# Optimization experiments

Hardware: AMD Instinct MI355X
Metric: run time of the kernel (lower is better)

## Reference

```python
import jax, jax.numpy as jnp
import numpy as np

DIM = 3072
HEADS = 24
HD = 128  # head_dim
RANK = 64
COND = 1024      # (512//8)*(512//8)*16//64
BLOCK = 2048     # main latent tokens
SEQ = BLOCK + COND
NIP = 64         # image_emb tokens
LORA_W = 1.0     # lora_weights[0]
ALPHA_SCALE = 1.0  # network_alpha / rank = 64/64
IP_SCALE = 1.0


def setup_inputs() -> dict:
    key = jax.random.key(0)
    ks = jax.random.split(key, 21)
    d = {}
    d["hidden_states"] = jax.random.normal(ks[0], (1, SEQ, DIM), jnp.float32)
    d["image_emb"] = jax.random.normal(ks[1], (1, NIP, DIM), jnp.float32)
    d["rope_cos"] = jax.random.uniform(ks[2], (SEQ, HD), jnp.float32)
    d["rope_sin"] = jax.random.uniform(ks[3], (SEQ, HD), jnp.float32)
    d["wq"] = jax.random.normal(ks[4], (DIM, DIM), jnp.float32) * 0.02
    d["bq"] = jax.random.normal(ks[5], (DIM,), jnp.float32) * 0.02
    d["wk"] = jax.random.normal(ks[6], (DIM, DIM), jnp.float32) * 0.02
    d["bk"] = jax.random.normal(ks[7], (DIM,), jnp.float32) * 0.02
    d["wv"] = jax.random.normal(ks[8], (DIM, DIM), jnp.float32) * 0.02
    d["bv"] = jax.random.normal(ks[9], (DIM,), jnp.float32) * 0.02
    d["norm_q_w"] = jax.random.uniform(ks[10], (HD,), jnp.float32, 0.5, 1.5)
    d["norm_k_w"] = jax.random.uniform(ks[11], (HD,), jnp.float32, 0.5, 1.5)
    d["q_down"] = jax.random.normal(ks[12], (RANK, DIM), jnp.float32) / RANK
    d["q_up"] = jax.random.normal(ks[13], (DIM, RANK), jnp.float32) * 0.02
    d["k_down"] = jax.random.normal(ks[14], (RANK, DIM), jnp.float32) / RANK
    d["k_up"] = jax.random.normal(ks[15], (DIM, RANK), jnp.float32) * 0.02
    d["v_down"] = jax.random.normal(ks[16], (RANK, DIM), jnp.float32) / RANK
    d["v_up"] = jax.random.normal(ks[17], (DIM, RANK), jnp.float32) * 0.02
    d["wk_ip"] = jax.random.normal(ks[18], (DIM, DIM), jnp.float32) * 0.02
    d["wv_ip"] = jax.random.normal(ks[19], (DIM, DIM), jnp.float32) * 0.02
    return d


def _rmsnorm(x, w, eps):
    v = jnp.mean(jnp.square(x), axis=-1, keepdims=True)
    y = x * jax.lax.rsqrt(v + eps)
    return y if w is None else y * w


def _heads(x, b):  # (B,S,DIM) -> (B,H,S,HD)
    return x.reshape(b, -1, HEADS, HD).transpose(0, 2, 1, 3)


def _rope(x, cos, sin):
    # diffusers apply_rotary_emb, use_real, unbind_dim=-1
    x1 = x[..., 0::2]
    x2 = x[..., 1::2]
    rot = jnp.stack([-x2, x1], axis=-1).reshape(x.shape)
    return x * cos[None, None] + rot * sin[None, None]


def _sdpa(q, k, v, bias=None):
    s = jnp.einsum("bhqd,bhkd->bhqk", q, k) / jnp.sqrt(jnp.float32(q.shape[-1]))
    if bias is not None:
        s = s + bias
    p = jax.nn.softmax(s, axis=-1)
    return jnp.einsum("bhqk,bhkd->bhqd", p, v)


def reference(hidden_states, image_emb, rope_cos, rope_sin,
              wq, bq, wk, bk, wv, bv, norm_q_w, norm_k_w,
              q_down, q_up, k_down, k_up, v_down, v_up, wk_ip, wv_ip):
    B = hidden_states.shape[0]

    # base QKV projections
    q = hidden_states @ wq.T + bq
    k = hidden_states @ wk.T + bk
    v = hidden_states @ wv.T + bv

    # original (pre-LoRA, pre-norm, pre-RoPE) query on the main block for IP attention
    original_query = _heads(hidden_states[:, :BLOCK] @ wq.T + bq, B)

    # masked LoRA add (n_loras=1): only tokens [BLOCK, BLOCK+COND) contribute
    pos = jnp.arange(SEQ)
    tok_mask = ((pos >= BLOCK) & (pos < BLOCK + COND)).astype(hidden_states.dtype)
    hm = hidden_states * tok_mask[None, :, None]
    q = q + LORA_W * ALPHA_SCALE * ((hm @ q_down.T) @ q_up.T)
    k = k + LORA_W * ALPHA_SCALE * ((hm @ k_down.T) @ k_up.T)
    v = v + LORA_W * ALPHA_SCALE * ((hm @ v_down.T) @ v_up.T)

    q = _heads(q, B)
    k = _heads(k, B)
    v = _heads(v, B)

    # per-head RMSNorm (attn.norm_q / attn.norm_k, eps=1e-6 in Flux)
    q = _rmsnorm(q, norm_q_w, 1e-6)
    k = _rmsnorm(k, norm_k_w, 1e-6)

    # IP-adapter cross attention with the original query
    ip_k = _rmsnorm(_heads(image_emb @ wk_ip.T, B), None, 1e-5)
    ip_v = _heads(image_emb @ wv_ip.T, B)
    ip_out = _sdpa(original_query, ip_k, ip_v)  # (B,H,BLOCK,HD)
    ip_out = ip_out.transpose(0, 2, 1, 3).reshape(B, -1, DIM)

    # RoPE on q/k
    q = _rope(q, rope_cos, rope_sin)
    k = _rope(k, rope_cos, rope_sin)

    # attention bias: main-block queries see everything; cond queries only their own block
    m = jnp.ones((SEQ, SEQ), jnp.float32)
    m = m.at[:BLOCK, :].set(0.0)
    m = m.at[BLOCK:BLOCK + COND, BLOCK:BLOCK + COND].set(0.0)
    bias = (m * -1e20)[None, None]

    out = _sdpa(q, k, v, bias)  # (B,H,SEQ,HD)
    out = out.transpose(0, 2, 1, 3).reshape(B, SEQ, DIM)

    main = out[:, :BLOCK, :] + IP_SCALE * ip_out
    return main
```

## Files before the change

### kernel.cpp

```cpp
#include <hip/hip_runtime.h>
#include <stdint.h>

#define DIM 3072
#define HEADS 24
#define HD 128
#define RANKN 64
#define CONDN 1024
#define BLK 2048
#define SEQN 3072
#define NIPN 64

typedef __attribute__((ext_vector_type(8))) short s8v;
typedef __attribute__((ext_vector_type(4))) float fx4;

static __device__ __forceinline__ unsigned short f2bf(float f){
  union{float f; unsigned u;} v; v.f=f;
  unsigned r = v.u + 0x7FFFu + ((v.u>>16)&1u);
  return (unsigned short)(r>>16);
}
static __device__ __forceinline__ float bf2f(unsigned short b){
  union{unsigned u; float f;} v; v.u = ((unsigned)b) << 16;
  return v.f;
}

#define GL16(g,l) __builtin_amdgcn_global_load_lds((const __attribute__((address_space(1))) void*)(g), (__attribute__((address_space(3))) void*)(l), 16, 0, 0)
#define MFMA(a,b,c) __builtin_amdgcn_mfma_f32_16x16x32_bf16((a),(b),(c),0,0,0)

__global__ __launch_bounds__(256) void cvt_f32_bf16(const float* __restrict__ src,
                                                    unsigned short* __restrict__ dst, int n4){
  int i = blockIdx.x*256 + threadIdx.x;
  if (i < n4){
    float4 v = ((const float4*)src)[i];
    ushort4 o;
    o.x = f2bf(v.x); o.y = f2bf(v.y); o.z = f2bf(v.z); o.w = f2bf(v.w);
    ((ushort4*)dst)[i] = o;
  }
}

__global__ __launch_bounds__(256) void cvt_w5(const float* __restrict__ s0, const float* __restrict__ s1,
                                              const float* __restrict__ s2, const float* __restrict__ s3,
                                              const float* __restrict__ s4,
                                              unsigned short* __restrict__ d0, unsigned short* __restrict__ d1,
                                              unsigned short* __restrict__ d2, unsigned short* __restrict__ d3,
                                              unsigned short* __restrict__ d4){
  int z = blockIdx.y;
  const float* src = z==0?s0:(z==1?s1:(z==2?s2:(z==3?s3:s4)));
  unsigned short* dst = z==0?d0:(z==1?d1:(z==2?d2:(z==3?d3:d4)));
  int i = blockIdx.x*256 + threadIdx.x;
  float4 v = ((const float4*)src)[i];
  ushort4 o;
  o.x = f2bf(v.x); o.y = f2bf(v.y); o.z = f2bf(v.z); o.w = f2bf(v.w);
  ((ushort4*)dst)[i] = o;
}

__global__ __launch_bounds__(256) void cvt_w4(const float* __restrict__ s0, const float* __restrict__ s1,
                                              const float* __restrict__ s2, const float* __restrict__ s3,
                                              unsigned short* __restrict__ d0, unsigned short* __restrict__ d1,
                                              unsigned short* __restrict__ d2, unsigned short* __restrict__ d3){
  int z = blockIdx.y;
  const float* src = z==0?s0:(z==1?s1:(z==2?s2:s3));
  unsigned short* dst = z==0?d0:(z==1?d1:(z==2?d2:d3));
  int i = blockIdx.x*256 + threadIdx.x;
  float4 v = ((const float4*)src)[i];
  ushort4 o;
  o.x = f2bf(v.x); o.y = f2bf(v.y); o.z = f2bf(v.z); o.w = f2bf(v.w);
  ((ushort4*)dst)[i] = o;
}

__global__ __launch_bounds__(256) void lora_down_g(const unsigned short* __restrict__ A,
                                                   const unsigned short* __restrict__ D0,
                                                   const unsigned short* __restrict__ D1,
                                                   unsigned short* __restrict__ outb){
  __shared__ unsigned short As[128*64];
  __shared__ unsigned short Bs[64*64];
  int tid = threadIdx.x, lane = tid & 63, w = tid >> 6;
  int l15 = lane & 15, l16 = lane >> 4;
  int z = blockIdx.z;
  int m0 = blockIdx.y * 128;
  const unsigned short* Dw = z ? D1 : D0;
  int wr = w * 32;
  fx4 acc[2][4] = {};
  for (int kt = 0; kt < DIM; kt += 64){
    #pragma unroll
    for (int i = 0; i < 4; i++){
      int p = i*256 + tid;
      int row = p >> 3, cc = p & 7;
      int gc = cc ^ (row & 7);
      GL16(A + (size_t)(m0+row)*DIM + kt + gc*8, As + p*8);
    }
    #pragma unroll
    for (int i = 0; i < 2; i++){
      int p = i*256 + tid;
      int row = p >> 3, cc = p & 7;
      int gc = cc ^ (row & 7);
      GL16(Dw + (size_t)row*DIM + kt + gc*8, Bs + p*8);
    }
    __syncthreads();
    #pragma unroll
    for (int kk = 0; kk < 2; kk++){
      s8v af[2], bfr[4];
      #pragma unroll
      for (int t = 0; t < 2; t++){
        int rowa = wr + t*16 + l15;
        int ca = (kk*4 + l16) ^ (rowa & 7);
        af[t] = *(const s8v*)(As + rowa*64 + ca*8);
      }
      #pragma unroll
      for (int t = 0; t < 4; t++){
        int rowb = t*16 + l15;
        int cb = (kk*4 + l16) ^ (rowb & 7);
        bfr[t] = *(const s8v*)(Bs + rowb*64 + cb*8);
      }
      #pragma unroll
      for (int mt = 0; mt < 2; mt++)
        #pragma unroll
        for (int nt = 0; nt < 4; nt++)
          acc[mt][nt] = MFMA(af[mt], bfr[nt], acc[mt][nt]);
    }
    __syncthreads();
  }
  #pragma unroll
  for (int mt = 0; mt < 2; mt++)
    #pragma unroll
    for (int j = 0; j < 4; j++){
      int row = m0 + wr + mt*16 + l16*4 + j;
      #pragma unroll
      for (int nt = 0; nt < 4; nt++){
        int col = nt*16 + l15;
        outb[((size_t)z*CONDN + row)*64 + col] = f2bf(acc[mt][nt][j]);
      }
    }
}

__global__ __launch_bounds__(512, 2) void gemm_256(
    const unsigned short* __restrict__ hs_bf,
    const unsigned short* __restrict__ ie_bf,
    const unsigned short* __restrict__ Wq,
    const unsigned short* __restrict__ Wk,
    const unsigned short* __restrict__ Wv,
    const unsigned short* __restrict__ Wik,
    const unsigned short* __restrict__ Wiv,
    const float* __restrict__ bq, const float* __restrict__ bk, const float* __restrict__ bv,
    const unsigned short* __restrict__ downb,
    const unsigned short* __restrict__ upk,
    const unsigned short* __restrict__ upv,
    unsigned short* __restrict__ qb, unsigned short* __restrict__ kb, unsigned short* __restrict__ vb,
    float* __restrict__ ipk_pre, float* __restrict__ ipv_pre)
{
  __shared__ unsigned short Ab[2][16384];
  __shared__ unsigned short Bb[2][16384];
  int tid = threadIdx.x, lane = tid & 63, w = tid >> 6;
  int wm = w >> 2, wn = w & 3;
  int l15 = lane & 15, l16 = lane >> 4;

  int b = blockIdx.x;
  int id = (b & 7) * 51 + (b >> 3);
  int z, mt, ntile;
  if (id < 96){ z = 0; mt = id / 12; ntile = id % 12; }
  else if (id < 240){ z = 1; int r = id - 96; mt = r / 12; ntile = r % 12; }
  else if (id < 384){ z = 2; int r = id - 240; mt = r / 12; ntile = r % 12; }
  else { z = 3; int r = id - 384; mt = r / 12; ntile = r % 12; }
  const bool is_ip = (z == 3);
  int z2 = is_ip ? mt : 0;
  int m0 = is_ip ? 0 : mt * 256;
  int n0 = ntile * 256;
  const unsigned short* A = is_ip ? ie_bf : hs_bf;
  const unsigned short* B = is_ip ? (z2 ? Wiv : Wik)
                                  : (z == 0 ? Wq : (z == 1 ? Wk : Wv));

  fx4 acc[8][4] = {};
  s8v af[8], bfr[8];

  auto stA = [&](int buf, int half, int kt){
    #pragma unroll
    for (int i = 0; i < 2; i++){
      int p = i*512 + tid;
      int row = p >> 3, cc = p & 7, gc = cc ^ (row & 7);
      int ar = m0 + half*128 + row;
      if (is_ip && ar > 63) ar = 63;
      GL16(A + (size_t)ar*DIM + kt + gc*8, &Ab[buf][half*8192 + p*8]);
    }
  };
  auto stB = [&](int buf, int half, int kt){
    #pragma unroll
    for (int i = 0; i < 2; i++){
      int p = i*512 + tid;
      int row = p >> 3, cc = p & 7, gc = cc ^ (row & 7);
      GL16(B + (size_t)(n0 + half*128 + row)*DIM + kt + gc*8, &Bb[buf][half*8192 + p*8]);
    }
  };
  auto rdA = [&](int buf, int m, int kk)->s8v{
    int rl = m*16 + l15;
    return *(const s8v*)(&Ab[buf][wm*8192 + rl*64 + ((kk*4 + l16) ^ (rl & 7))*8]);
  };
  auto rdB = [&](int buf, int n, int kk)->s8v{
    int rB = wn*64 + n*16 + l15;
    return *(const s8v*)(&Bb[buf][(rB >> 7)*8192 + (rB & 127)*64 + ((kk*4 + l16) ^ (rB & 7))*8]);
  };

  stA(0,0,0); stA(0,1,0); stB(0,0,0); stB(0,1,0);

  const int NT = DIM / 64;
  for (int t = 0; t < NT; t++){
    int cur = t & 1, nxt = cur ^ 1;
    bool pf = (t + 1 < NT);
    if (pf){
      int kt1 = (t + 1) * 64;
      stA(nxt, 0, kt1); stA(nxt, 1, kt1);
      stB(nxt, 0, kt1); stB(nxt, 1, kt1);
      asm volatile("s_waitcnt vmcnt(8)" ::: "memory");
    } else {
      asm volatile("s_waitcnt vmcnt(0)" ::: "memory");
    }
    __builtin_amdgcn_s_barrier();

    #pragma unroll
    for (int m = 0; m < 4; m++){ af[m*2] = rdA(cur,m,0); af[m*2+1] = rdA(cur,m,1); }
    #pragma unroll
    for (int n = 0; n < 2; n++){ bfr[n*2] = rdB(cur,n,0); bfr[n*2+1] = rdB(cur,n,1); }
    __builtin_amdgcn_s_setprio(1);
    #pragma unroll
    for (int m = 0; m < 4; m++)
      #pragma unroll
      for (int n = 0; n < 2; n++){
        acc[m][n] = MFMA(af[m*2],   bfr[n*2],   acc[m][n]);
        acc[m][n] = MFMA(af[m*2+1], bfr[n*2+1], acc[m][n]);
      }
    __builtin_amdgcn_s_setprio(0);
    #pragma unroll
    for (int n = 2; n < 4; n++){ bfr[n*2] = rdB(cur,n,0); bfr[n*2+1] = rdB(cur,n,1); }
    __builtin_amdgcn_s_setprio(1);
    #pragma unroll
    for (int m = 0; m < 4; m++)
      #pragma unroll
      for (int n = 2; n < 4; n++){
        acc[m][n] = MFMA(af[m*2],   bfr[n*2],   acc[m][n]);
        acc[m][n] = MFMA(af[m*2+1], bfr[n*2+1], acc[m][n]);
      }
    __builtin_amdgcn_s_setprio(0);
    #pragma unroll
    for (int m = 4; m < 8; m++){ af[(m-4)*2] = rdA(cur,m,0); af[(m-4)*2+1] = rdA(cur,m,1); }
    __builtin_amdgcn_s_setprio(1);
    #pragma unroll
    for (int m = 4; m < 8; m++)
      #pragma unroll
      for (int n = 2; n < 4; n++){
        acc[m][n] = MFMA(af[(m-4)*2],   bfr[n*2],   acc[m][n]);
        acc[m][n] = MFMA(af[(m-4)*2+1], bfr[n*2+1], acc[m][n]);
      }
    #pragma unroll
    for (int m = 4; m < 8; m++)
      #pragma unroll
      for (int n = 0; n < 2; n++){
        acc[m][n] = MFMA(af[(m-4)*2],   bfr[n*2],   acc[m][n]);
        acc[m][n] = MFMA(af[(m-4)*2+1], bfr[n*2+1], acc[m][n]);
      }
    __builtin_amdgcn_s_setprio(0);
    __builtin_amdgcn_s_barrier();
  }

  if (is_ip){
    float* outp = z2 ? ipv_pre : ipk_pre;
    if (wm == 0){
      #pragma unroll
      for (int m = 0; m < 4; m++)
        #pragma unroll
        for (int j = 0; j < 4; j++){
          int row = m*16 + l16*4 + j;
          #pragma unroll
          for (int n = 0; n < 4; n++)
            outp[(size_t)row*DIM + n0 + wn*64 + n*16 + l15] = acc[m][n][j];
        }
    }
    return;
  }

  if (z >= 1 && m0 >= BLK){
    const unsigned short* dwn = downb + (size_t)(z-1)*CONDN*64 + (size_t)(m0 - BLK)*64;
    const unsigned short* up  = (z == 1) ? upk : upv;
    #pragma unroll
    for (int i = 0; i < 4; i++){
      int p = i*512 + tid;
      int row = p >> 3, cc = p & 7, gc = cc ^ (row & 7);
      GL16(dwn + (size_t)row*64 + gc*8, &Ab[0][p*8]);
      GL16(up + (size_t)(n0 + row)*64 + gc*8, &Bb[0][p*8]);
    }
    asm volatile("s_waitcnt vmcnt(0)" ::: "memory");
    __builtin_amdgcn_s_barrier();
    #pragma unroll
    for (int kk = 0; kk < 2; kk++){
      s8v aL[8], bL[4];
      #pragma unroll
      for (int m = 0; m < 8; m++){
        int rA = wm*128 + m*16 + l15;
        aL[m] = *(const s8v*)(&Ab[0][rA*64 + ((kk*4 + l16) ^ (rA & 7))*8]);
      }
      #pragma unroll
      for (int n = 0; n < 4; n++){
        int rB = wn*64 + n*16 + l15;
        bL[n] = *(const s8v*)(&Bb[0][rB*64 + ((kk*4 + l16) ^ (rB & 7))*8]);
      }
      #pragma unroll
      for (int m = 0; m < 8; m++)
        #pragma unroll
        for (int n = 0; n < 4; n++)
          acc[m][n] = MFMA(aL[m], bL[n], acc[m][n]);
    }
  }

  {
    const float* bias = z == 0 ? bq : (z == 1 ? bk : bv);
    unsigned short* C = z == 0 ? qb : (z == 1 ? kb : vb);
    float bv4[4];
    #pragma unroll
    for (int n = 0; n < 4; n++) bv4[n] = bias[n0 + wn*64 + n*16 + l15];
    #pragma unroll
    for (int m = 0; m < 8; m++)
      #pragma unroll
      for (int j = 0; j < 4; j++){
        int row = m0 + wm*128 + m*16 + l16*4 + j;
        unsigned short* crow = C + (size_t)row*DIM;
        #pragma unroll
        for (int n = 0; n < 4; n++)
          crow[n0 + wn*64 + n*16 + l15] = f2bf(acc[m][n][j] + bv4[n]);
      }
  }
}

__global__ __launch_bounds__(256) void norm_rope(const unsigned short* __restrict__ src,
                                                 unsigned short* __restrict__ dst,
                                                 const float* __restrict__ wt,
                                                 const float* __restrict__ rc,
                                                 const float* __restrict__ rs,
                                                 int S, float qscale){
  int tid = threadIdx.x, lane = tid & 63, w = tid >> 6;
  int r = blockIdx.x*4 + w;
  int pos = r % S, h = r / S;
  const unsigned short* x = src + (size_t)pos*DIM + h*HD;
  ushort2 xv2 = *(const ushort2*)(x + 2*lane);
  float x0 = bf2f(xv2.x), x1 = bf2f(xv2.y);
  float ss = x0*x0 + x1*x1;
  #pragma unroll
  for (int o = 1; o < 64; o <<= 1) ss += __shfl_xor(ss, o);
  float rr = rsqrtf(ss*(1.f/128.f) + 1e-6f);
  float y0 = x0*rr*wt[2*lane], y1 = x1*rr*wt[2*lane+1];
  float2 cv = *(const float2*)(rc + (size_t)pos*HD + 2*lane);
  float2 sv = *(const float2*)(rs + (size_t)pos*HD + 2*lane);
  float o0 = (y0*cv.x - y1*sv.x)*qscale;
  float o1 = (y1*cv.y + y0*sv.y)*qscale;
  ushort2 ov; ov.x = f2bf(o0); ov.y = f2bf(o1);
  *(ushort2*)(dst + ((size_t)h*S + pos)*HD + 2*lane) = ov;
}

__global__ __launch_bounds__(256) void ipk_norm_bf(const float* __restrict__ src,
                                                   unsigned short* __restrict__ dst){
  int tid = threadIdx.x, lane = tid & 63, w = tid >> 6;
  int r = blockIdx.x*4 + w;
  int pos = r / HEADS, h = r % HEADS;
  const float* x = src + (size_t)pos*DIM + h*HD;
  float2 xv = *(const float2*)(x + 2*lane);
  float ss = xv.x*xv.x + xv.y*xv.y;
  #pragma unroll
  for (int o = 1; o < 64; o <<= 1) ss += __shfl_xor(ss, o);
  float rr = rsqrtf(ss*(1.f/128.f) + 1e-5f);
  ushort2 ov; ov.x = f2bf(xv.x*rr); ov.y = f2bf(xv.y*rr);
  *(ushort2*)(dst + ((size_t)h*NIPN + pos)*HD + 2*lane) = ov;
}

__global__ __launch_bounds__(256) void ipv_transpose(const float* __restrict__ ipv,
                                                     unsigned short* __restrict__ vt){
  int h = blockIdx.x, tid = threadIdx.x;
  #pragma unroll
  for (int i = 0; i < 32; i++){
    int idx = i*256 + tid;
    int d = idx >> 6, key = idx & 63;
    vt[((size_t)h*HD + d)*64 + key] = f2bf(ipv[(size_t)key*DIM + h*HD + d]);
  }
}

__global__ __launch_bounds__(256) void v_transpose(const unsigned short* __restrict__ v,
                                                   unsigned short* __restrict__ Vt){
  __shared__ unsigned short t[64][137];
  int h = blockIdx.y, p0 = blockIdx.x*64, tid = threadIdx.x;
  int dcol = tid & 127, prow2 = tid >> 7;
  #pragma unroll
  for (int i = 0; i < 32; i++){
    int pos = i*2 + prow2;
    t[pos][dcol] = v[(size_t)(p0+pos)*DIM + h*HD + dcol];
  }
  __syncthreads();
  int pos = tid & 63, dbase = tid >> 6;
  #pragma unroll
  for (int i = 0; i < 32; i++){
    int d = i*4 + dbase;
    Vt[((size_t)h*HD + d)*SEQN + p0 + pos] = t[pos][d];
  }
}

__global__ __launch_bounds__(256) void ip_attn_m(const unsigned short* __restrict__ qb,
                                                 const unsigned short* __restrict__ ipk_bf,
                                                 const unsigned short* __restrict__ ipv_t,
                                                 float* __restrict__ out){
  __shared__ unsigned short Ks[64*HD];
  __shared__ unsigned short Vs[HD*64];
  __shared__ unsigned short Ps[4][16*64];
  int tid = threadIdx.x, lane = tid & 63, w = tid >> 6;
  int l15 = lane & 15, l16 = lane >> 4;
  int h = blockIdx.y;
  int q0 = blockIdx.x*64 + w*16;
  const unsigned short* Kh = ipk_bf + (size_t)h*NIPN*HD;
  const unsigned short* Vh = ipv_t + (size_t)h*HD*NIPN;

  #pragma unroll
  for (int i = 0; i < 4; i++){
    int p = i*256 + tid;
    int row = p >> 4, cc = p & 15;
    int gc = cc ^ (row & 7);
    GL16(Kh + (size_t)row*HD + gc*8, Ks + p*8);
  }
  #pragma unroll
  for (int i = 0; i < 4; i++){
    int p = i*256 + tid;
    int row = p >> 3, cc = p & 7;
    int gc = cc ^ (row & 7);
    GL16(Vh + (size_t)row*64 + gc*8, Vs + p*8);
  }

  s8v qf[4];
  #pragma unroll
  for (int kf = 0; kf < 4; kf++)
    qf[kf] = *(const s8v*)(qb + (size_t)(q0 + l15)*DIM + h*HD + kf*32 + l16*8);
  __syncthreads();

  fx4 s[4] = {};
  #pragma unroll
  for (int ct = 0; ct < 4; ct++){
    #pragma unroll
    for (int kk = 0; kk < 4; kk++){
      int row = ct*16 + l15;
      int c = (kk*4 + l16) ^ (row & 7);
      s8v b = *(const s8v*)(Ks + row*HD + c*8);
      s[ct] = MFMA(qf[kk], b, s[ct]);
    }
  }
  const float SC = 0.08838834764831845f;
  float lrow[4];
  #pragma unroll
  for (int j = 0; j < 4; j++){
    #pragma unroll
    for (int ct = 0; ct < 4; ct++) s[ct][j] *= SC;
    float v = fmaxf(fmaxf(s[0][j], s[1][j]), fmaxf(s[2][j], s[3][j]));
    #pragma unroll
    for (int o2 = 1; o2 < 16; o2 <<= 1) v = fmaxf(v, __shfl_xor(v, o2));
    float sum = 0.f;
    #pragma unroll
    for (int ct = 0; ct < 4; ct++){
      float p = __expf(s[ct][j] - v);
      s[ct][j] = p;
      sum += p;
    }
    #pragma unroll
    for (int o2 = 1; o2 < 16; o2 <<= 1) sum += __shfl_xor(sum, o2);
    lrow[j] = sum;
  }

  #pragma unroll
  for (int ct = 0; ct < 4; ct++)
    #pragma unroll
    for (int j = 0; j < 4; j++){
      int row = l16*4 + j;
      int cidx = ct*16 + l15;
      Ps[w][row*64 + (((cidx>>3) ^ (row&7))<<3) + (cidx&7)] = f2bf(s[ct][j]);
    }
  asm volatile("s_waitcnt lgkmcnt(0)" ::: "memory");
  s8v pa[2];
  #pragma unroll
  for (int kk = 0; kk < 2; kk++){
    int c = (kk*4 + l16) ^ (l15 & 7);
    pa[kk] = *(const s8v*)(&Ps[w][l15*64 + c*8]);
  }
  fx4 o[8] = {};
  #pragma unroll
  for (int nt = 0; nt < 8; nt++){
    #pragma unroll
    for (int kk = 0; kk < 2; kk++){
      int row = nt*16 + l15;
      int c = (kk*4 + l16) ^ (row & 7);
      s8v bv = *(const s8v*)(Vs + row*64 + c*8);
      o[nt] = MFMA(pa[kk], bv, o[nt]);
    }
  }
  #pragma unroll
  for (int nt = 0; nt < 8; nt++)
    #pragma unroll
    for (int j = 0; j < 4; j++){
      int row = q0 + l16*4 + j;
      int d = nt*16 + l15;
      out[(size_t)row*DIM + h*HD + d] = o[nt][j] / lrow[j];
    }
}

#define QB 128
#define KVB 64
#define PSTR 72
__global__ __launch_bounds__(512, 4) void flash_attn_split(const unsigned short* __restrict__ Qn,
                                                           const unsigned short* __restrict__ Kn,
                                                           const unsigned short* __restrict__ Vt,
                                                           float* __restrict__ po0,
                                                           float* __restrict__ po1,
                                                           float* __restrict__ pm,
                                                           float* __restrict__ pl){
  __shared__ unsigned short Ks[KVB*HD];
  __shared__ unsigned short Vs[HD*KVB];
  __shared__ unsigned short Ps[8][16*PSTR];
  int tid = threadIdx.x, lane = tid & 63, w = tid >> 6;
  int l15 = lane & 15, l16 = lane >> 4;
  int b = blockIdx.x;
  int swz = (b & 7) * 96 + (b >> 3);
  int sp = swz / 384;
  int rem = swz - sp*384;
  int h = rem >> 4;
  int qt = rem & 15;
  int q0 = qt*QB + w*16;
  const unsigned short* Qh = Qn + (size_t)h*BLK*HD;
  const unsigned short* Kh = Kn + (size_t)h*SEQN*HD;
  const unsigned short* Vh = Vt + (size_t)h*HD*SEQN;
  const int kvbase = sp * (SEQN/2);
  const int NT = (SEQN/2) / KVB;

  s8v qf[4];
  #pragma unroll
  for (int kf = 0; kf < 4; kf++)
    qf[kf] = *(const s8v*)(Qh + (size_t)(q0 + l15)*HD + kf*32 + l16*8);

  fx4 o[8] = {};
  float mrow[4], lrow[4];
  #pragma unroll
  for (int j = 0; j < 4; j++){ mrow[j] = -1e30f; lrow[j] = 0.f; }

  for (int t = 0; t < NT; t++){
    int kv0 = kvbase + t*KVB;
    #pragma unroll
    for (int i = 0; i < 2; i++){
      int p = i*512 + tid;
      int row = p >> 4, cc = p & 15;
      int gc = cc ^ (row & 7);
      GL16(Kh + (size_t)(kv0+row)*HD + gc*8, Ks + p*8);
    }
    #pragma unroll
    for (int i = 0; i < 2; i++){
      int p = i*512 + tid;
      int row = p >> 3, cc = p & 7;
      int gc = cc ^ (row & 7);
      GL16(Vh + (size_t)row*SEQN + kv0 + gc*8, Vs + p*8);
    }
    __syncthreads();

    fx4 s[4] = {};
    #pragma unroll
    for (int ct = 0; ct < 4; ct++){
      #pragma unroll
      for (int kk = 0; kk < 4; kk++){
        int row = ct*16 + l15;
        int c = (kk*4 + l16) ^ (row & 7);
        s8v bb = *(const s8v*)(Ks + row*HD + c*8);
        s[ct] = MFMA(qf[kk], bb, s[ct]);
      }
    }
    float pmax[4], rssum[4];
    #pragma unroll
    for (int j = 0; j < 4; j++){
      float v = fmaxf(fmaxf(s[0][j], s[1][j]), fmaxf(s[2][j], s[3][j]));
      #pragma unroll
      for (int o2 = 1; o2 < 16; o2 <<= 1) v = fmaxf(v, __shfl_xor(v, o2));
      pmax[j] = v;
      rssum[j] = 0.f;
    }
    float need = 0.f;
    #pragma unroll
    for (int j = 0; j < 4; j++) need = fmaxf(need, pmax[j] - mrow[j]);
    if (__any(need > 8.f)){
      float alpha[4];
      #pragma unroll
      for (int j = 0; j < 4; j++){
        float mnew = fmaxf(mrow[j], pmax[j]);
        alpha[j] = __expf(mrow[j] - mnew);
        mrow[j] = mnew;
      }
      #pragma unroll
      for (int nt = 0; nt < 8; nt++)
        #pragma unroll
        for (int j = 0; j < 4; j++) o[nt][j] *= alpha[j];
      #pragma unroll
      for (int j = 0; j < 4; j++) lrow[j] *= alpha[j];
    }
    #pragma unroll
    for (int ct = 0; ct < 4; ct++)
      #pragma unroll
      for (int j = 0; j < 4; j++){
        float p = __expf(s[ct][j] - mrow[j]);
        s[ct][j] = p;
        rssum[j] += p;
      }
    #pragma unroll
    for (int j = 0; j < 4; j++){
      #pragma unroll
      for (int o2 = 1; o2 < 16; o2 <<= 1) rssum[j] += __shfl_xor(rssum[j], o2);
      lrow[j] += rssum[j];
    }

    #pragma unroll
    for (int ct = 0; ct < 4; ct++)
      #pragma unroll
      for (int j = 0; j < 4; j++){
        int row = l16*4 + j;
        int cidx = ct*16 + l15;
        Ps[w][row*PSTR + cidx] = f2bf(s[ct][j]);
      }
    asm volatile("s_waitcnt lgkmcnt(0)" ::: "memory");
    s8v pa[2];
    #pragma unroll
    for (int kk = 0; kk < 2; kk++)
      pa[kk] = *(const s8v*)(&Ps[w][l15*PSTR + (kk*4 + l16)*8]);
    #pragma unroll
    for (int nt = 0; nt < 8; nt++){
      #pragma unroll
      for (int kk = 0; kk < 2; kk++){
        int row = nt*16 + l15;
        int c = (kk*4 + l16) ^ (row & 7);
        s8v bvv = *(const s8v*)(Vs + row*KVB + c*8);
        o[nt] = MFMA(pa[kk], bvv, o[nt]);
      }
    }
    __syncthreads();
  }

  float* pop = sp ? po1 : po0;
  #pragma unroll
  for (int nt = 0; nt < 8; nt++)
    #pragma unroll
    for (int j = 0; j < 4; j++){
      int row = q0 + l16*4 + j;
      int d = nt*16 + l15;
      pop[((size_t)h*BLK + row)*HD + d] = o[nt][j];
    }
  if (l15 == 0){
    #pragma unroll
    for (int j = 0; j < 4; j++){
      int row = q0 + l16*4 + j;
      pm[(size_t)sp*HEADS*BLK + h*BLK + row] = mrow[j];
      pl[(size_t)sp*HEADS*BLK + h*BLK + row] = lrow[j];
    }
  }
}

__global__ __launch_bounds__(256) void flash_merge(const float* __restrict__ po0,
                                                   const float* __restrict__ po1,
                                                   const float* __restrict__ pm,
                                                   const float* __restrict__ pl,
                                                   float* __restrict__ out){
  int tid = threadIdx.x, lane = tid & 63, w = tid >> 6;
  int r = blockIdx.x*4 + w;
  int h = r >> 11, pos = r & 2047;
  float m0 = pm[r], m1 = pm[HEADS*BLK + r];
  float l0 = pl[r], l1 = pl[HEADS*BLK + r];
  float mx = fmaxf(m0, m1);
  float a0 = __expf(m0 - mx), a1 = __expf(m1 - mx);
  float li = 1.f / (l0*a0 + l1*a1);
  float s0 = a0*li, s1 = a1*li;
  size_t base = ((size_t)h*BLK + pos)*HD + 2*lane;
  float2 x0 = *(const float2*)(po0 + base);
  float2 x1 = *(const float2*)(po1 + base);
  float* op = out + (size_t)pos*DIM + h*HD + 2*lane;
  float2 cv = *(const float2*)op;
  cv.x += x0.x*s0 + x1.x*s1;
  cv.y += x0.y*s0 + x1.y*s1;
  *(float2*)op = cv;
}

extern "C" void kernel_launch(void* const* d_in, const int* in_sizes, int n_in,
                              void* d_out, int out_size, void* d_ws, size_t ws_size,
                              hipStream_t stream){
  (void)in_sizes; (void)n_in; (void)out_size;
  const float* hs       = (const float*)d_in[0];
  const float* image_emb= (const float*)d_in[1];
  const float* rope_cos = (const float*)d_in[2];
  const float* rope_sin = (const float*)d_in[3];
  const float* wq = (const float*)d_in[4];
  const float* bq = (const float*)d_in[5];
  const float* wk = (const float*)d_in[6];
  const float* bk = (const float*)d_in[7];
  const float* wv = (const float*)d_in[8];
  const float* bv = (const float*)d_in[9];
  const float* norm_q_w = (const float*)d_in[10];
  const float* norm_k_w = (const float*)d_in[11];
  const float* k_down = (const float*)d_in[14];
  const float* k_up   = (const float*)d_in[15];
  const float* v_down = (const float*)d_in[16];
  const float* v_up   = (const float*)d_in[17];
  const float* wk_ip  = (const float*)d_in[18];
  const float* wv_ip  = (const float*)d_in[19];
  float* out = (float*)d_out;

  char* ws = (char*)d_ws;
  size_t off = 0;
  auto alloc = [&](size_t bytes){ void* p = ws + off; off += (bytes + 255) & ~(size_t)255; return p; };
  unsigned short* hs_bf = (unsigned short*)alloc((size_t)SEQN*DIM*2);
  unsigned short* ie_bf = (unsigned short*)alloc((size_t)NIPN*DIM*2);
  unsigned short* w_bf[5];
  for (int i = 0; i < 5; i++) w_bf[i] = (unsigned short*)alloc((size_t)DIM*DIM*2);
  unsigned short* lw_bf[4];
  for (int i = 0; i < 4; i++) lw_bf[i] = (unsigned short*)alloc((size_t)RANKN*DIM*2);
  unsigned short* downb = (unsigned short*)alloc((size_t)2*CONDN*RANKN*2);
  unsigned short* qb = (unsigned short*)alloc((size_t)BLK*DIM*2);
  unsigned short* kb = (unsigned short*)alloc((size_t)SEQN*DIM*2);
  unsigned short* vb = (unsigned short*)alloc((size_t)SEQN*DIM*2);
  float* ipk_pre = (float*)alloc((size_t)NIPN*DIM*4);
  float* ipv_pre = (float*)alloc((size_t)NIPN*DIM*4);
  unsigned short* ipk_bf = (unsigned short*)alloc((size_t)HEADS*NIPN*HD*2);
  unsigned short* ipv_t  = (unsigned short*)alloc((size_t)HEADS*HD*NIPN*2);
  float* po0 = (float*)alloc((size_t)HEADS*BLK*HD*4);
  float* po1 = (float*)alloc((size_t)HEADS*BLK*HD*4);
  float* pm  = (float*)alloc((size_t)2*HEADS*BLK*4);
  float* pl  = (float*)alloc((size_t)2*HEADS*BLK*4);
  if (off > ws_size) return;

  unsigned short* Qn = w_bf[0];
  unsigned short* Kn = w_bf[1];
  unsigned short* Vt = w_bf[2];

  int n4;
  n4 = SEQN*DIM/4;
  cvt_f32_bf16<<<(n4+255)/256, 256, 0, stream>>>(hs, hs_bf, n4);
  n4 = NIPN*DIM/4;
  cvt_f32_bf16<<<(n4+255)/256, 256, 0, stream>>>(image_emb, ie_bf, n4);

  cvt_w5<<<dim3(DIM*DIM/4/256, 5), 256, 0, stream>>>(wq, wk, wv, wk_ip, wv_ip,
      w_bf[0], w_bf[1], w_bf[2], w_bf[3], w_bf[4]);
  cvt_w4<<<dim3(RANKN*DIM/4/256, 4), 256, 0, stream>>>(k_down, v_down, k_up, v_up,
      lw_bf[0], lw_bf[1], lw_bf[2], lw_bf[3]);

  lora_down_g<<<dim3(1, CONDN/128, 2), 256, 0, stream>>>(hs_bf + (size_t)BLK*DIM,
      lw_bf[0], lw_bf[1], downb);

  gemm_256<<<408, 512, 0, stream>>>(hs_bf, ie_bf,
      w_bf[0], w_bf[1], w_bf[2], w_bf[3], w_bf[4],
      bq, bk, bv, downb, lw_bf[2], lw_bf[3],
      qb, kb, vb, ipk_pre, ipv_pre);

  ipk_norm_bf<<<(NIPN*HEADS)/4, 256, 0, stream>>>(ipk_pre, ipk_bf);
  ipv_transpose<<<HEADS, 256, 0, stream>>>(ipv_pre, ipv_t);

  const float SC = 0.08838834764831845f;
  norm_rope<<<(BLK*HEADS)/4, 256, 0, stream>>>(qb, Qn, norm_q_w, rope_cos, rope_sin, BLK, SC);
  norm_rope<<<(SEQN*HEADS)/4, 256, 0, stream>>>(kb, Kn, norm_k_w, rope_cos, rope_sin, SEQN, 1.0f);
  v_transpose<<<dim3(SEQN/64, HEADS), 256, 0, stream>>>(vb, Vt);

  ip_attn_m<<<dim3(BLK/64, HEADS), 256, 0, stream>>>(qb, ipk_bf, ipv_t, out);
  flash_attn_split<<<768, 512, 0, stream>>>(Qn, Kn, Vt, po0, po1, pm, pl);
  flash_merge<<<(HEADS*BLK)/4, 256, 0, stream>>>(po0, po1, pm, pl, out);
}
```

Baseline: 528.4 us.

## Double GEMM wavefronts per block with smaller per-wave 64x64 tiles

The fused QKV/IP projection GEMM goes from 512 to 1024 threads per block. Each of the 16 waves now computes a 64x64 sub-tile instead of 128x64, which halves the accumulator registers per wave and simplifies the k-loop to a plain two-step LDS-read/MFMA sequence. The staggered A/B fragment scheduling is removed, and the global-to-LDS staging and vmcnt wait are adjusted to match. The aim is more waves in flight to hide latency. In exchange, the ratio of LDS reads to MFMAs gets worse, and the aggressive launch bounds may force register spills.

```diff
diff --git a/kernel.cpp b/kernel.cpp
--- a/kernel.cpp
+++ b/kernel.cpp
@@ -132,7 +132,7 @@
     }
 }
 
-__global__ __launch_bounds__(512, 2) void gemm_256(
+__global__ __launch_bounds__(1024, 4) void gemm_256(
     const unsigned short* __restrict__ hs_bf,
     const unsigned short* __restrict__ ie_bf,
     const unsigned short* __restrict__ Wq,
@@ -168,37 +168,36 @@
   const unsigned short* B = is_ip ? (z2 ? Wiv : Wik)
                                   : (z == 0 ? Wq : (z == 1 ? Wk : Wv));
 
-  fx4 acc[8][4] = {};
-  s8v af[8], bfr[8];
-
-  auto stA = [&](int buf, int half, int kt){
+  fx4 acc[4][4] = {};
+
+  auto stA = [&](int buf, int kt){
     #pragma unroll
     for (int i = 0; i < 2; i++){
-      int p = i*512 + tid;
+      int p = i*1024 + tid;
       int row = p >> 3, cc = p & 7, gc = cc ^ (row & 7);
-      int ar = m0 + half*128 + row;
+      int ar = m0 + row;
       if (is_ip && ar > 63) ar = 63;
-      GL16(A + (size_t)ar*DIM + kt + gc*8, &Ab[buf][half*8192 + p*8]);
+      GL16(A + (size_t)ar*DIM + kt + gc*8, &Ab[buf][p*8]);
     }
   };
-  auto stB = [&](int buf, int half, int kt){
+  auto stB = [&](int buf, int kt){
     #pragma unroll
     for (int i = 0; i < 2; i++){
-      int p = i*512 + tid;
+      int p = i*1024 + tid;
       int row = p >> 3, cc = p & 7, gc = cc ^ (row & 7);
-      GL16(B + (size_t)(n0 + half*128 + row)*DIM + kt + gc*8, &Bb[buf][half*8192 + p*8]);
+      GL16(B + (size_t)(n0 + row)*DIM + kt + gc*8, &Bb[buf][p*8]);
     }
   };
   auto rdA = [&](int buf, int m, int kk)->s8v{
-    int rl = m*16 + l15;
-    return *(const s8v*)(&Ab[buf][wm*8192 + rl*64 + ((kk*4 + l16) ^ (rl & 7))*8]);
+    int rl = wm*64 + m*16 + l15;
+    return *(const s8v*)(&Ab[buf][rl*64 + (((kk*4 + l16) ^ (rl & 7))*8)]);
   };
   auto rdB = [&](int buf, int n, int kk)->s8v{
     int rB = wn*64 + n*16 + l15;
-    return *(const s8v*)(&Bb[buf][(rB >> 7)*8192 + (rB & 127)*64 + ((kk*4 + l16) ^ (rB & 7))*8]);
+    return *(const s8v*)(&Bb[buf][rB*64 + (((kk*4 + l16) ^ (rB & 7))*8)]);
   };
 
-  stA(0,0,0); stA(0,1,0); stB(0,0,0); stB(0,1,0);
+  stA(0, 0); stB(0, 0);
 
   const int NT = DIM / 64;
   for (int t = 0; t < NT; t++){
@@ -206,56 +205,28 @@
     bool pf = (t + 1 < NT);
     if (pf){
       int kt1 = (t + 1) * 64;
-      stA(nxt, 0, kt1); stA(nxt, 1, kt1);
-      stB(nxt, 0, kt1); stB(nxt, 1, kt1);
-      asm volatile("s_waitcnt vmcnt(8)" ::: "memory");
+      stA(nxt, kt1); stB(nxt, kt1);
+      asm volatile("s_waitcnt vmcnt(4)" ::: "memory");
     } else {
       asm volatile("s_waitcnt vmcnt(0)" ::: "memory");
     }
     __builtin_amdgcn_s_barrier();
 
     #pragma unroll
-    for (int m = 0; m < 4; m++){ af[m*2] = rdA(cur,m,0); af[m*2+1] = rdA(cur,m,1); }
-    #pragma unroll
-    for (int n = 0; n < 2; n++){ bfr[n*2] = rdB(cur,n,0); bfr[n*2+1] = rdB(cur,n,1); }
-    __builtin_amdgcn_s_setprio(1);
-    #pragma unroll
-    for (int m = 0; m < 4; m++)
-      #pragma unroll
-      for (int n = 0; n < 2; n++){
-        acc[m][n] = MFMA(af[m*2],   bfr[n*2],   acc[m][n]);
-        acc[m][n] = MFMA(af[m*2+1], bfr[n*2+1], acc[m][n]);
-      }
-    __builtin_amdgcn_s_setprio(0);
-    #pragma unroll
-    for (int n = 2; n < 4; n++){ bfr[n*2] = rdB(cur,n,0); bfr[n*2+1] = rdB(cur,n,1); }
-    __builtin_amdgcn_s_setprio(1);
-    #pragma unroll
-    for (int m = 0; m < 4; m++)
-      #pragma unroll
-      for (int n = 2; n < 4; n++){
-        acc[m][n] = MFMA(af[m*2],   bfr[n*2],   acc[m][n]);
-        acc[m][n] = MFMA(af[m*2+1], bfr[n*2+1], acc[m][n]);
-      }
-    __builtin_amdgcn_s_setprio(0);
-    #pragma unroll
-    for (int m = 4; m < 8; m++){ af[(m-4)*2] = rdA(cur,m,0); af[(m-4)*2+1] = rdA(cur,m,1); }
-    __builtin_amdgcn_s_setprio(1);
-    #pragma unroll
-    for (int m = 4; m < 8; m++)
-      #pragma unroll
-      for (int n = 2; n < 4; n++){
-        acc[m][n] = MFMA(af[(m-4)*2],   bfr[n*2],   acc[m][n]);
-        acc[m][n] = MFMA(af[(m-4)*2+1], bfr[n*2+1], acc[m][n]);
-      }
-    #pragma unroll
-    for (int m = 4; m < 8; m++)
-      #pragma unroll
-      for (int n = 0; n < 2; n++){
-        acc[m][n] = MFMA(af[(m-4)*2],   bfr[n*2],   acc[m][n]);
-        acc[m][n] = MFMA(af[(m-4)*2+1], bfr[n*2+1], acc[m][n]);
-      }
-    __builtin_amdgcn_s_setprio(0);
+    for (int kk = 0; kk < 2; kk++){
+      s8v af[4], bfr[4];
+      #pragma unroll
+      for (int m = 0; m < 4; m++) af[m] = rdA(cur, m, kk);
+      #pragma unroll
+      for (int n = 0; n < 4; n++) bfr[n] = rdB(cur, n, kk);
+      __builtin_amdgcn_s_setprio(1);
+      #pragma unroll
+      for (int m = 0; m < 4; m++)
+        #pragma unroll
+        for (int n = 0; n < 4; n++)
+          acc[m][n] = MFMA(af[m], bfr[n], acc[m][n]);
+      __builtin_amdgcn_s_setprio(0);
+    }
     __builtin_amdgcn_s_barrier();
   }
 
@@ -279,8 +250,8 @@
     const unsigned short* dwn = downb + (size_t)(z-1)*CONDN*64 + (size_t)(m0 - BLK)*64;
     const unsigned short* up  = (z == 1) ? upk : upv;
     #pragma unroll
-    for (int i = 0; i < 4; i++){
-      int p = i*512 + tid;
+    for (int i = 0; i < 2; i++){
+      int p = i*1024 + tid;
       int row = p >> 3, cc = p & 7, gc = cc ^ (row & 7);
       GL16(dwn + (size_t)row*64 + gc*8, &Ab[0][p*8]);
       GL16(up + (size_t)(n0 + row)*64 + gc*8, &Bb[0][p*8]);
@@ -289,19 +260,19 @@
     __builtin_amdgcn_s_barrier();
     #pragma unroll
     for (int kk = 0; kk < 2; kk++){
-      s8v aL[8], bL[4];
-      #pragma unroll
-      for (int m = 0; m < 8; m++){
-        int rA = wm*128 + m*16 + l15;
-        aL[m] = *(const s8v*)(&Ab[0][rA*64 + ((kk*4 + l16) ^ (rA & 7))*8]);
+      s8v aL[4], bL[4];
+      #pragma unroll
+      for (int m = 0; m < 4; m++){
+        int rA = wm*64 + m*16 + l15;
+        aL[m] = *(const s8v*)(&Ab[0][rA*64 + (((kk*4 + l16) ^ (rA & 7))*8)]);
       }
       #pragma unroll
       for (int n = 0; n < 4; n++){
         int rB = wn*64 + n*16 + l15;
-        bL[n] = *(const s8v*)(&Bb[0][rB*64 + ((kk*4 + l16) ^ (rB & 7))*8]);
-      }
-      #pragma unroll
-      for (int m = 0; m < 8; m++)
+        bL[n] = *(const s8v*)(&Bb[0][rB*64 + (((kk*4 + l16) ^ (rB & 7))*8)]);
+      }
+      #pragma unroll
+      for (int m = 0; m < 4; m++)
         #pragma unroll
         for (int n = 0; n < 4; n++)
           acc[m][n] = MFMA(aL[m], bL[n], acc[m][n]);
@@ -315,10 +286,10 @@
     #pragma unroll
     for (int n = 0; n < 4; n++) bv4[n] = bias[n0 + wn*64 + n*16 + l15];
     #pragma unroll
-    for (int m = 0; m < 8; m++)
+    for (int m = 0; m < 4; m++)
       #pragma unroll
       for (int j = 0; j < 4; j++){
-        int row = m0 + wm*128 + m*16 + l16*4 + j;
+        int row = m0 + wm*64 + m*16 + l16*4 + j;
         unsigned short* crow = C + (size_t)row*DIM;
         #pragma unroll
         for (int n = 0; n < 4; n++)
@@ -743,7 +714,7 @@
   lora_down_g<<<dim3(1, CONDN/128, 2), 256, 0, stream>>>(hs_bf + (size_t)BLK*DIM,
       lw_bf[0], lw_bf[1], downb);
 
-  gemm_256<<<408, 512, 0, stream>>>(hs_bf, ie_bf,
+  gemm_256<<<408, 1024, 0, stream>>>(hs_bf, ie_bf,
       w_bf[0], w_bf[1], w_bf[2], w_bf[3], w_bf[4],
       bq, bk, bv, downb, lw_bf[2], lw_bf[3],
       qb, kb, vb, ipk_pre, ipv_pre);
```

After: 534.3 us. No clear change (+1.1%).
